# Optimization experiments

Hardware: AMD Instinct MI355X
Metric: run time of the kernel (lower is better)

The kernel has to match this reference:

```python
import jax, jax.numpy as jnp
import numpy as np

N_NODES = 100000
N_EDGES = 1600000
N_FEAT = 32
HIDDEN = 96
N_GRAPHS = 2048


def setup_inputs() -> dict:
    key = jax.random.key(0)
    ks = jax.random.split(key, 16)
    x = jax.random.normal(ks[0], (N_NODES, N_FEAT), dtype=jnp.float32)
    edge_index = jax.random.randint(ks[1], (2, N_EDGES), 0, N_NODES, dtype=jnp.int64)
    batch = jnp.sort(jax.random.randint(ks[2], (N_NODES,), 0, N_GRAPHS, dtype=jnp.int64))

    def glorot(k, shape):
        lim = np.sqrt(6.0 / (shape[0] + shape[1]))
        return jax.random.uniform(k, shape, dtype=jnp.float32, minval=-lim, maxval=lim)

    return {
        "x": x, "edge_index": edge_index, "batch": batch,
        "W1": glorot(ks[3], (N_FEAT, HIDDEN)), "b1": jnp.zeros((HIDDEN,), jnp.float32),
        "W2": glorot(ks[4], (HIDDEN, HIDDEN)), "b2": jnp.zeros((HIDDEN,), jnp.float32),
        "W3": glorot(ks[5], (HIDDEN, HIDDEN)), "b3": jnp.zeros((HIDDEN,), jnp.float32),
        "W4": glorot(ks[6], (HIDDEN, HIDDEN)), "b4": jnp.zeros((HIDDEN,), jnp.float32),
        "Wf1": glorot(ks[7], (HIDDEN, 32)), "bf1": jnp.zeros((32,), jnp.float32),
        "Wf2": glorot(ks[8], (32, 1)), "bf2": jnp.zeros((1,), jnp.float32),
    }


def _gcn_norm(edge_index, num_nodes):
    # PyG GCNConv default: add self-loops, symmetric normalization D^-1/2 (A+I) D^-1/2
    loops = jnp.arange(num_nodes, dtype=edge_index.dtype)
    src = jnp.concatenate([edge_index[0], loops])
    dst = jnp.concatenate([edge_index[1], loops])
    deg = jax.ops.segment_sum(jnp.ones_like(dst, dtype=jnp.float32), dst, num_segments=num_nodes)
    dinv = jnp.where(deg > 0, jax.lax.rsqrt(jnp.where(deg > 0, deg, 1.0)), 0.0)
    norm = dinv[src] * dinv[dst]  # [E + N]
    return src, dst, norm


def _gcn_conv(x, src, dst, norm, W, b, num_nodes):
    xw = x @ W                      # [N, out]
    msg = xw[src] * norm[:, None]   # [E+N, out] gather + scale
    out = jax.ops.segment_sum(msg, dst, num_segments=num_nodes)  # scatter-add
    return out + b


def reference(x, edge_index, batch, W1, b1, W2, b2, W3, b3, W4, b4, Wf1, bf1, Wf2, bf2):
    n = x.shape[0]
    src, dst, norm = _gcn_norm(edge_index, n)
    h = jax.nn.relu(_gcn_conv(x, src, dst, norm, W1, b1, n))
    h = jax.nn.relu(_gcn_conv(h, src, dst, norm, W2, b2, n))
    h = jax.nn.relu(_gcn_conv(h, src, dst, norm, W3, b3, n))
    h = jax.nn.relu(_gcn_conv(h, src, dst, norm, W4, b4, n))
    g = jax.ops.segment_sum(h, batch, num_segments=N_GRAPHS)  # global_add_pool [G, 96]
    g = jax.nn.relu(g @ Wf1 + bf1)
    return g @ Wf2 + bf2  # [G, 1]
```

## Files before the change

kernel.cpp:

```cpp
#include <hip/hip_runtime.h>
#include <hip/hip_fp16.h>


#define HIDDEN 96

__device__ inline float4 h4_to_f4(uint2 u) {
    __half2 a = *reinterpret_cast<__half2*>(&u.x);
    __half2 b = *reinterpret_cast<__half2*>(&u.y);
    float2 fa = __half22float2(a), fb = __half22float2(b);
    return make_float4(fa.x, fa.y, fb.x, fb.y);
}

__device__ inline uint2 f4_to_h4(float4 v) {
    __half2 a = __float22half2_rn(make_float2(v.x, v.y));
    __half2 b = __float22half2_rn(make_float2(v.z, v.w));
    uint2 u;
    u.x = *reinterpret_cast<unsigned*>(&a);
    u.y = *reinterpret_cast<unsigned*>(&b);
    return u;
}

__device__ inline int pad8(int c) { return (c + 7) & ~7; }

__global__ __launch_bounds__(256) void zero_int_kernel(int* p, int n) {
    int i = blockIdx.x * 256 + threadIdx.x;
    if (i < n) p[i] = 0;
}

__global__ __launch_bounds__(256) void zero_kernel(float* p, int n) {
    int i = blockIdx.x * 256 + threadIdx.x;
    if (i < n) p[i] = 0.0f;
}

__global__ __launch_bounds__(256) void cast_h_kernel(const float4* __restrict__ in,
                                                     uint2* __restrict__ out, int n4) {
    int i = blockIdx.x * 256 + threadIdx.x;
    if (i < n4) out[i] = f4_to_h4(in[i]);
}

__global__ __launch_bounds__(256) void deg_pos_kernel(const int* __restrict__ dst,
                                                      int* __restrict__ cnt,
                                                      int* __restrict__ epos, int E) {
    int e = blockIdx.x * 256 + threadIdx.x;
    if (e < E) epos[e] = atomicAdd(&cnt[dst[e]], 1);
}

__global__ __launch_bounds__(256) void dinv_kernel(const int* __restrict__ cnt,
                                                   float* __restrict__ dinv, int n) {
    int i = blockIdx.x * 256 + threadIdx.x;
    if (i < n) dinv[i] = rsqrtf((float)(cnt[i] + 1));
}

__global__ __launch_bounds__(256) void scan_reduce_kernel(const int* __restrict__ cnt,
                                                          int* __restrict__ bsum, int N) {
    __shared__ int s[256];
    int b = blockIdx.x, tid = threadIdx.x;
    int base = b * 1024;
    int v = 0;
    for (int j = tid; j < 1024; j += 256) {
        int i = base + j;
        v += (i < N) ? pad8(cnt[i]) : 0;
    }
    s[tid] = v;
    __syncthreads();
    for (int off = 128; off > 0; off >>= 1) {
        if (tid < off) s[tid] += s[tid + off];
        __syncthreads();
    }
    if (tid == 0) bsum[b] = s[0];
}

__global__ __launch_bounds__(128) void scan_bsum_kernel(int* __restrict__ bsum, int nb) {
    __shared__ int s[128];
    int tid = threadIdx.x;
    int v = (tid < nb) ? bsum[tid] : 0;
    s[tid] = v;
    __syncthreads();
    for (int off = 1; off < 128; off <<= 1) {
        int t = (tid >= off) ? s[tid - off] : 0;
        __syncthreads();
        s[tid] += t;
        __syncthreads();
    }
    if (tid < nb) bsum[tid] = s[tid] - v;
}

__global__ __launch_bounds__(256) void scan_write_kernel(const int* __restrict__ cnt,
                                                         const int* __restrict__ bsum,
                                                         int* __restrict__ rowptr, int N) {
    __shared__ int ts[256];
    int b = blockIdx.x, tid = threadIdx.x;
    int base = b * 1024 + tid * 4;
    int v0 = (base + 0 < N) ? pad8(cnt[base + 0]) : 0;
    int v1 = (base + 1 < N) ? pad8(cnt[base + 1]) : 0;
    int v2 = (base + 2 < N) ? pad8(cnt[base + 2]) : 0;
    int v3 = (base + 3 < N) ? pad8(cnt[base + 3]) : 0;
    int sum = v0 + v1 + v2 + v3;
    ts[tid] = sum;
    __syncthreads();
    for (int off = 1; off < 256; off <<= 1) {
        int t = (tid >= off) ? ts[tid - off] : 0;
        __syncthreads();
        ts[tid] += t;
        __syncthreads();
    }
    int excl = bsum[b] + ts[tid] - sum;
    if (base + 0 <= N) rowptr[base + 0] = excl;
    if (base + 1 <= N) rowptr[base + 1] = excl + v0;
    if (base + 2 <= N) rowptr[base + 2] = excl + v0 + v1;
    if (base + 3 <= N) rowptr[base + 3] = excl + v0 + v1 + v2;
}

__global__ __launch_bounds__(256) void fill_csr_kernel(const int* __restrict__ src,
                                                       const int* __restrict__ dst,
                                                       const int* __restrict__ epos,
                                                       const float* __restrict__ dinv,
                                                       const int* __restrict__ rowptr,
                                                       int* __restrict__ col,
                                                       float* __restrict__ val, int E) {
    int e = blockIdx.x * 256 + threadIdx.x;
    if (e >= E) return;
    int s = src[e];
    int d = dst[e];
    int idx = rowptr[d] + epos[e];
    col[idx] = s;
    val[idx] = dinv[s] * dinv[d];
}

template <int K, bool RELU, bool BIAS>
__global__ __launch_bounds__(256) void gemm_kernel(const uint2* __restrict__ X,
                                                   const float* __restrict__ W,
                                                   const float* __restrict__ b,
                                                   uint2* __restrict__ Y, int n) {
    __shared__ float wlds[K * HIDDEN];
    for (int idx = threadIdx.x; idx < K * HIDDEN; idx += 256) wlds[idx] = W[idx];
    __syncthreads();

    int row = blockIdx.x * 256 + threadIdx.x;
    if (row >= n) return;

    float4 acc[24];
#pragma unroll
    for (int j = 0; j < 24; j++) acc[j] = make_float4(0.f, 0.f, 0.f, 0.f);

    const float4* wl4 = reinterpret_cast<const float4*>(wlds);
    const uint2* xrow = X + (size_t)row * (K / 4);

    for (int k0 = 0; k0 < K; k0 += 4) {
        float4 xv = h4_to_f4(xrow[k0 >> 2]);
        if (RELU) {
            xv.x = fmaxf(xv.x, 0.f); xv.y = fmaxf(xv.y, 0.f);
            xv.z = fmaxf(xv.z, 0.f); xv.w = fmaxf(xv.w, 0.f);
        }
#pragma unroll
        for (int kk = 0; kk < 4; kk++) {
            float xs = (kk == 0) ? xv.x : (kk == 1) ? xv.y : (kk == 2) ? xv.z : xv.w;
#pragma unroll
            for (int j = 0; j < 24; j++) {
                float4 w = wl4[(k0 + kk) * 24 + j];
                acc[j].x += xs * w.x;
                acc[j].y += xs * w.y;
                acc[j].z += xs * w.z;
                acc[j].w += xs * w.w;
            }
        }
    }

    uint2* y2 = Y + (size_t)row * 24;
#pragma unroll
    for (int j = 0; j < 24; j++) {
        if (BIAS) {
            float4 bb = reinterpret_cast<const float4*>(b)[j];
            acc[j].x += bb.x; acc[j].y += bb.y; acc[j].z += bb.z; acc[j].w += bb.w;
        }
        y2[j] = f4_to_h4(acc[j]);
    }
}

template <int TPN, bool POOL, bool BIAS>
__global__ __launch_bounds__(256) void aggregate_kernel(const uint2* __restrict__ xwh,
                                                        const int* __restrict__ rowptr,
                                                        const int* __restrict__ col,
                                                        const float* __restrict__ val,
                                                        const float* __restrict__ dinv,
                                                        const float* __restrict__ b,
                                                        uint2* __restrict__ out,
                                                        const int* __restrict__ batch,
                                                        float* __restrict__ gpool, int n) {
    unsigned t = blockIdx.x * 256 + threadIdx.x;
    unsigned i = t / (unsigned)TPN, q = t % (unsigned)TPN;
    if (i >= (unsigned)n) return;

    float dv = dinv[i];
    float s = dv * dv;
    float4 self = h4_to_f4(xwh[i * TPN + q]);
    float4 acc = make_float4(s * self.x, s * self.y, s * self.z, s * self.w);
    if (BIAS) {
        float4 bb = reinterpret_cast<const float4*>(b)[q];
        acc.x += bb.x; acc.y += bb.y; acc.z += bb.z; acc.w += bb.w;
    }

    int e = rowptr[i], end = rowptr[i + 1];
    for (; e < end; e += 8) {
        int4 ca = *reinterpret_cast<const int4*>(col + e);
        int4 cb = *reinterpret_cast<const int4*>(col + e + 4);
        float4 wa = *reinterpret_cast<const float4*>(val + e);
        float4 wb = *reinterpret_cast<const float4*>(val + e + 4);
        uint2 u0 = xwh[(unsigned)ca.x * TPN + q];
        uint2 u1 = xwh[(unsigned)ca.y * TPN + q];
        uint2 u2 = xwh[(unsigned)ca.z * TPN + q];
        uint2 u3 = xwh[(unsigned)ca.w * TPN + q];
        uint2 u4 = xwh[(unsigned)cb.x * TPN + q];
        uint2 u5 = xwh[(unsigned)cb.y * TPN + q];
        uint2 u6 = xwh[(unsigned)cb.z * TPN + q];
        uint2 u7 = xwh[(unsigned)cb.w * TPN + q];
        float4 v0 = h4_to_f4(u0), v1 = h4_to_f4(u1);
        float4 v2 = h4_to_f4(u2), v3 = h4_to_f4(u3);
        float4 v4 = h4_to_f4(u4), v5 = h4_to_f4(u5);
        float4 v6 = h4_to_f4(u6), v7 = h4_to_f4(u7);
        acc.x += wa.x * v0.x + wa.y * v1.x + wa.z * v2.x + wa.w * v3.x
               + wb.x * v4.x + wb.y * v5.x + wb.z * v6.x + wb.w * v7.x;
        acc.y += wa.x * v0.y + wa.y * v1.y + wa.z * v2.y + wa.w * v3.y
               + wb.x * v4.y + wb.y * v5.y + wb.z * v6.y + wb.w * v7.y;
        acc.z += wa.x * v0.z + wa.y * v1.z + wa.z * v2.z + wa.w * v3.z
               + wb.x * v4.z + wb.y * v5.z + wb.z * v6.z + wb.w * v7.z;
        acc.w += wa.x * v0.w + wa.y * v1.w + wa.z * v2.w + wa.w * v3.w
               + wb.x * v4.w + wb.y * v5.w + wb.z * v6.w + wb.w * v7.w;
    }

    if (POOL) {
        float* o = gpool + (size_t)batch[i] * (TPN * 4);
        unsigned fo = q * 4u;
        atomicAdd(o + fo + 0, fmaxf(acc.x, 0.f));
        atomicAdd(o + fo + 1, fmaxf(acc.y, 0.f));
        atomicAdd(o + fo + 2, fmaxf(acc.z, 0.f));
        atomicAdd(o + fo + 3, fmaxf(acc.w, 0.f));
    } else {
        out[i * TPN + q] = f4_to_h4(acc);
    }
}

__global__ __launch_bounds__(64) void mlp_kernel(const float* __restrict__ g,
                                                 const float* __restrict__ Wf1,
                                                 const float* __restrict__ bf1,
                                                 const float* __restrict__ Wf2,
                                                 const float* __restrict__ bf2,
                                                 float* __restrict__ out, int G) {
    __shared__ float gs[HIDDEN];
    __shared__ float hid[32];
    int blk = blockIdx.x;
    int lane = threadIdx.x;
    for (int idx = lane; idx < HIDDEN; idx += 64) gs[idx] = g[(size_t)blk * HIDDEN + idx];
    __syncthreads();
    if (lane < 32) {
        float a = bf1[lane];
        for (int k = 0; k < HIDDEN; k++) a = fmaf(gs[k], Wf1[k * 32 + lane], a);
        hid[lane] = fmaxf(a, 0.f);
    }
    __syncthreads();
    if (lane == 0) {
        float o = bf2[0];
        for (int k = 0; k < 32; k++) o = fmaf(hid[k], Wf2[k], o);
        out[blk] = o;
    }
}

extern "C" void kernel_launch(void* const* d_in, const int* in_sizes, int n_in,
                              void* d_out, int out_size, void* d_ws, size_t ws_size,
                              hipStream_t stream) {
    const float* x     = (const float*)d_in[0];
    const int*   ei    = (const int*)d_in[1];
    const int*   batch = (const int*)d_in[2];
    const float* W1 = (const float*)d_in[3];  const float* b1 = (const float*)d_in[4];
    const float* W2 = (const float*)d_in[5];  const float* b2 = (const float*)d_in[6];
    const float* W3 = (const float*)d_in[7];  const float* b3 = (const float*)d_in[8];
    const float* W4 = (const float*)d_in[9];  const float* b4 = (const float*)d_in[10];
    const float* Wf1 = (const float*)d_in[11]; const float* bf1 = (const float*)d_in[12];
    const float* Wf2 = (const float*)d_in[13]; const float* bf2 = (const float*)d_in[14];
    float* out = (float*)d_out;

    int N = in_sizes[0] / 32;
    int E = in_sizes[1] / 2;
    int G = out_size;
    const int* src = ei;
    const int* dst = ei + E;
    int Emax = E + 8 * N;

    char* ws = (char*)d_ws;
    size_t off = 0;
    auto alloc = [&](size_t bytes) -> void* {
        void* p = (void*)(ws + off);
        off += (bytes + 255) & ~(size_t)255;
        return p;
    };
    int*   degcnt = (int*)alloc((size_t)N * 4);
    float* dinv   = (float*)alloc((size_t)N * 4);
    int*   rowptr = (int*)alloc((size_t)(N + 1) * 4);
    int*   bsum   = (int*)alloc((size_t)128 * 4);
    int*   col    = (int*)alloc((size_t)Emax * 4);
    float* val    = (float*)alloc((size_t)Emax * 4);
    int*   epos   = (int*)alloc((size_t)E * 4);
    uint2* xh     = (uint2*)alloc((size_t)N * 32 * 2);
    uint2* aggXh  = (uint2*)alloc((size_t)N * 32 * 2);
    uint2* bufB   = (uint2*)alloc((size_t)N * HIDDEN * 2);
    uint2* bufH   = (uint2*)alloc((size_t)N * HIDDEN * 2);
    float* gbuf   = (float*)alloc((size_t)G * HIDDEN * 4);
    (void)ws_size;

    int gN   = (N + 255) / 256;
    int gE   = (E + 255) / 256;
    int gEm  = (Emax + 255) / 256;
    int gAgg32 = (int)(((long long)N * 8 + 255) / 256);
    int gAgg96 = (int)(((long long)N * 24 + 255) / 256);
    int nb   = (N + 1023) / 1024;

    zero_int_kernel<<<gN, 256, 0, stream>>>(degcnt, N);
    zero_int_kernel<<<gEm, 256, 0, stream>>>(col, Emax);
    zero_kernel<<<gEm, 256, 0, stream>>>(val, Emax);
    deg_pos_kernel<<<gE, 256, 0, stream>>>(dst, degcnt, epos, E);
    dinv_kernel<<<gN, 256, 0, stream>>>(degcnt, dinv, N);
    scan_reduce_kernel<<<nb, 256, 0, stream>>>(degcnt, bsum, N);
    scan_bsum_kernel<<<1, 128, 0, stream>>>(bsum, nb);
    scan_write_kernel<<<nb, 256, 0, stream>>>(degcnt, bsum, rowptr, N);
    fill_csr_kernel<<<gE, 256, 0, stream>>>(src, dst, epos, dinv, rowptr, col, val, E);

    cast_h_kernel<<<(N * 8 + 255) / 256, 256, 0, stream>>>(
        reinterpret_cast<const float4*>(x), xh, N * 8);
    aggregate_kernel<8, false, false><<<gAgg32, 256, 0, stream>>>(
        xh, rowptr, col, val, dinv, nullptr, aggXh, nullptr, nullptr, N);
    gemm_kernel<32, false, true><<<gN, 256, 0, stream>>>(aggXh, W1, b1, bufB, N);

    gemm_kernel<96, true, false><<<gN, 256, 0, stream>>>(bufB, W2, nullptr, bufH, N);
    aggregate_kernel<24, false, true><<<gAgg96, 256, 0, stream>>>(
        bufH, rowptr, col, val, dinv, b2, bufB, nullptr, nullptr, N);

    gemm_kernel<96, true, false><<<gN, 256, 0, stream>>>(bufB, W3, nullptr, bufH, N);
    aggregate_kernel<24, false, true><<<gAgg96, 256, 0, stream>>>(
        bufH, rowptr, col, val, dinv, b3, bufB, nullptr, nullptr, N);

    zero_kernel<<<(G * HIDDEN + 255) / 256, 256, 0, stream>>>(gbuf, G * HIDDEN);
    gemm_kernel<96, true, false><<<gN, 256, 0, stream>>>(bufB, W4, nullptr, bufH, N);
    aggregate_kernel<24, true, true><<<gAgg96, 256, 0, stream>>>(
        bufH, rowptr, col, val, dinv, b4, nullptr, batch, gbuf, N);

    mlp_kernel<<<G, 64, 0, stream>>>(gbuf, Wf1, bf1, Wf2, bf2, out, G);
}
```

Baseline: 696.5 us.

## Widen aggregate gathers to 16-byte loads and pad CSR rows to 4

Result: slower. 922.0 us (+32.4%).

```diff
diff --git a/kernel.cpp b/kernel.cpp
--- a/kernel.cpp
+++ b/kernel.cpp
@@ -20,7 +20,7 @@
     return u;
 }
 
-__device__ inline int pad8(int c) { return (c + 7) & ~7; }
+__device__ inline int pad4(int c) { return (c + 3) & ~3; }
 
 __global__ __launch_bounds__(256) void zero_int_kernel(int* p, int n) {
     int i = blockIdx.x * 256 + threadIdx.x;
@@ -59,7 +59,7 @@
     int v = 0;
     for (int j = tid; j < 1024; j += 256) {
         int i = base + j;
-        v += (i < N) ? pad8(cnt[i]) : 0;
+        v += (i < N) ? pad4(cnt[i]) : 0;
     }
     s[tid] = v;
     __syncthreads();
@@ -91,10 +91,10 @@
     __shared__ int ts[256];
     int b = blockIdx.x, tid = threadIdx.x;
     int base = b * 1024 + tid * 4;
-    int v0 = (base + 0 < N) ? pad8(cnt[base + 0]) : 0;
-    int v1 = (base + 1 < N) ? pad8(cnt[base + 1]) : 0;
-    int v2 = (base + 2 < N) ? pad8(cnt[base + 2]) : 0;
-    int v3 = (base + 3 < N) ? pad8(cnt[base + 3]) : 0;
+    int v0 = (base + 0 < N) ? pad4(cnt[base + 0]) : 0;
+    int v1 = (base + 1 < N) ? pad4(cnt[base + 1]) : 0;
+    int v2 = (base + 2 < N) ? pad4(cnt[base + 2]) : 0;
+    int v3 = (base + 3 < N) ? pad4(cnt[base + 3]) : 0;
     int sum = v0 + v1 + v2 + v3;
     ts[tid] = sum;
     __syncthreads();
@@ -178,13 +178,13 @@
 }
 
 template <int TPN, bool POOL, bool BIAS>
-__global__ __launch_bounds__(256) void aggregate_kernel(const uint2* __restrict__ xwh,
+__global__ __launch_bounds__(256) void aggregate_kernel(const uint4* __restrict__ xwh,
                                                         const int* __restrict__ rowptr,
                                                         const int* __restrict__ col,
                                                         const float* __restrict__ val,
                                                         const float* __restrict__ dinv,
                                                         const float* __restrict__ b,
-                                                        uint2* __restrict__ out,
+                                                        uint4* __restrict__ out,
                                                         const int* __restrict__ batch,
                                                         float* __restrict__ gpool, int n) {
     unsigned t = blockIdx.x * 256 + threadIdx.x;
@@ -193,50 +193,53 @@
 
     float dv = dinv[i];
     float s = dv * dv;
-    float4 self = h4_to_f4(xwh[i * TPN + q]);
-    float4 acc = make_float4(s * self.x, s * self.y, s * self.z, s * self.w);
+    uint4 su = xwh[i * TPN + q];
+    float4 sa = h4_to_f4(make_uint2(su.x, su.y));
+    float4 sb = h4_to_f4(make_uint2(su.z, su.w));
+    float4 accA = make_float4(s * sa.x, s * sa.y, s * sa.z, s * sa.w);
+    float4 accB = make_float4(s * sb.x, s * sb.y, s * sb.z, s * sb.w);
     if (BIAS) {
-        float4 bb = reinterpret_cast<const float4*>(b)[q];
-        acc.x += bb.x; acc.y += bb.y; acc.z += bb.z; acc.w += bb.w;
+        const float4* b4 = reinterpret_cast<const float4*>(b);
+        float4 ba = b4[q * 2 + 0], bb = b4[q * 2 + 1];
+        accA.x += ba.x; accA.y += ba.y; accA.z += ba.z; accA.w += ba.w;
+        accB.x += bb.x; accB.y += bb.y; accB.z += bb.z; accB.w += bb.w;
     }
 
     int e = rowptr[i], end = rowptr[i + 1];
-    for (; e < end; e += 8) {
-        int4 ca = *reinterpret_cast<const int4*>(col + e);
-        int4 cb = *reinterpret_cast<const int4*>(col + e + 4);
-        float4 wa = *reinterpret_cast<const float4*>(val + e);
-        float4 wb = *reinterpret_cast<const float4*>(val + e + 4);
-        uint2 u0 = xwh[(unsigned)ca.x * TPN + q];
-        uint2 u1 = xwh[(unsigned)ca.y * TPN + q];
-        uint2 u2 = xwh[(unsigned)ca.z * TPN + q];
-        uint2 u3 = xwh[(unsigned)ca.w * TPN + q];
-        uint2 u4 = xwh[(unsigned)cb.x * TPN + q];
-        uint2 u5 = xwh[(unsigned)cb.y * TPN + q];
-        uint2 u6 = xwh[(unsigned)cb.z * TPN + q];
-        uint2 u7 = xwh[(unsigned)cb.w * TPN + q];
-        float4 v0 = h4_to_f4(u0), v1 = h4_to_f4(u1);
-        float4 v2 = h4_to_f4(u2), v3 = h4_to_f4(u3);
-        float4 v4 = h4_to_f4(u4), v5 = h4_to_f4(u5);
-        float4 v6 = h4_to_f4(u6), v7 = h4_to_f4(u7);
-        acc.x += wa.x * v0.x + wa.y * v1.x + wa.z * v2.x + wa.w * v3.x
-               + wb.x * v4.x + wb.y * v5.x + wb.z * v6.x + wb.w * v7.x;
-        acc.y += wa.x * v0.y + wa.y * v1.y + wa.z * v2.y + wa.w * v3.y
-               + wb.x * v4.y + wb.y * v5.y + wb.z * v6.y + wb.w * v7.y;
-        acc.z += wa.x * v0.z + wa.y * v1.z + wa.z * v2.z + wa.w * v3.z
-               + wb.x * v4.z + wb.y * v5.z + wb.z * v6.z + wb.w * v7.z;
-        acc.w += wa.x * v0.w + wa.y * v1.w + wa.z * v2.w + wa.w * v3.w
-               + wb.x * v4.w + wb.y * v5.w + wb.z * v6.w + wb.w * v7.w;
+    for (; e < end; e += 4) {
+        int4 c4 = *reinterpret_cast<const int4*>(col + e);
+        float4 w4 = *reinterpret_cast<const float4*>(val + e);
+        uint4 u0 = xwh[(unsigned)c4.x * TPN + q];
+        uint4 u1 = xwh[(unsigned)c4.y * TPN + q];
+        uint4 u2 = xwh[(unsigned)c4.z * TPN + q];
+        uint4 u3 = xwh[(unsigned)c4.w * TPN + q];
+        float4 a0 = h4_to_f4(make_uint2(u0.x, u0.y)), b0 = h4_to_f4(make_uint2(u0.z, u0.w));
+        float4 a1 = h4_to_f4(make_uint2(u1.x, u1.y)), b1 = h4_to_f4(make_uint2(u1.z, u1.w));
+        float4 a2 = h4_to_f4(make_uint2(u2.x, u2.y)), b2 = h4_to_f4(make_uint2(u2.z, u2.w));
+        float4 a3 = h4_to_f4(make_uint2(u3.x, u3.y)), b3 = h4_to_f4(make_uint2(u3.z, u3.w));
+        accA.x += w4.x * a0.x + w4.y * a1.x + w4.z * a2.x + w4.w * a3.x;
+        accA.y += w4.x * a0.y + w4.y * a1.y + w4.z * a2.y + w4.w * a3.y;
+        accA.z += w4.x * a0.z + w4.y * a1.z + w4.z * a2.z + w4.w * a3.z;
+        accA.w += w4.x * a0.w + w4.y * a1.w + w4.z * a2.w + w4.w * a3.w;
+        accB.x += w4.x * b0.x + w4.y * b1.x + w4.z * b2.x + w4.w * b3.x;
+        accB.y += w4.x * b0.y + w4.y * b1.y + w4.z * b2.y + w4.w * b3.y;
+        accB.z += w4.x * b0.z + w4.y * b1.z + w4.z * b2.z + w4.w * b3.z;
+        accB.w += w4.x * b0.w + w4.y * b1.w + w4.z * b2.w + w4.w * b3.w;
     }
 
     if (POOL) {
-        float* o = gpool + (size_t)batch[i] * (TPN * 4);
-        unsigned fo = q * 4u;
-        atomicAdd(o + fo + 0, fmaxf(acc.x, 0.f));
-        atomicAdd(o + fo + 1, fmaxf(acc.y, 0.f));
-        atomicAdd(o + fo + 2, fmaxf(acc.z, 0.f));
-        atomicAdd(o + fo + 3, fmaxf(acc.w, 0.f));
+        float* o = gpool + (size_t)batch[i] * (TPN * 8) + q * 8u;
+        atomicAdd(o + 0, fmaxf(accA.x, 0.f));
+        atomicAdd(o + 1, fmaxf(accA.y, 0.f));
+        atomicAdd(o + 2, fmaxf(accA.z, 0.f));
+        atomicAdd(o + 3, fmaxf(accA.w, 0.f));
+        atomicAdd(o + 4, fmaxf(accB.x, 0.f));
+        atomicAdd(o + 5, fmaxf(accB.y, 0.f));
+        atomicAdd(o + 6, fmaxf(accB.z, 0.f));
+        atomicAdd(o + 7, fmaxf(accB.w, 0.f));
     } else {
-        out[i * TPN + q] = f4_to_h4(acc);
+        uint2 ha = f4_to_h4(accA), hb = f4_to_h4(accB);
+        out[i * TPN + q] = make_uint4(ha.x, ha.y, hb.x, hb.y);
     }
 }
 
@@ -284,7 +287,7 @@
     int G = out_size;
     const int* src = ei;
     const int* dst = ei + E;
-    int Emax = E + 8 * N;
+    int Emax = E + 4 * N;
 
     char* ws = (char*)d_ws;
     size_t off = 0;
@@ -301,17 +304,17 @@
     float* val    = (float*)alloc((size_t)Emax * 4);
     int*   epos   = (int*)alloc((size_t)E * 4);
     uint2* xh     = (uint2*)alloc((size_t)N * 32 * 2);
-    uint2* aggXh  = (uint2*)alloc((size_t)N * 32 * 2);
-    uint2* bufB   = (uint2*)alloc((size_t)N * HIDDEN * 2);
-    uint2* bufH   = (uint2*)alloc((size_t)N * HIDDEN * 2);
+    uint4* aggXh  = (uint4*)alloc((size_t)N * 32 * 2);
+    uint4* bufB   = (uint4*)alloc((size_t)N * HIDDEN * 2);
+    uint4* bufH   = (uint4*)alloc((size_t)N * HIDDEN * 2);
     float* gbuf   = (float*)alloc((size_t)G * HIDDEN * 4);
     (void)ws_size;
 
     int gN   = (N + 255) / 256;
     int gE   = (E + 255) / 256;
     int gEm  = (Emax + 255) / 256;
-    int gAgg32 = (int)(((long long)N * 8 + 255) / 256);
-    int gAgg96 = (int)(((long long)N * 24 + 255) / 256);
+    int gAgg32 = (int)(((long long)N * 4 + 255) / 256);
+    int gAgg96 = (int)(((long long)N * 12 + 255) / 256);
     int nb   = (N + 1023) / 1024;
 
     zero_int_kernel<<<gN, 256, 0, stream>>>(degcnt, N);
@@ -326,21 +329,30 @@
 
     cast_h_kernel<<<(N * 8 + 255) / 256, 256, 0, stream>>>(
         reinterpret_cast<const float4*>(x), xh, N * 8);
-    aggregate_kernel<8, false, false><<<gAgg32, 256, 0, stream>>>(
-        xh, rowptr, col, val, dinv, nullptr, aggXh, nullptr, nullptr, N);
-    gemm_kernel<32, false, true><<<gN, 256, 0, stream>>>(aggXh, W1, b1, bufB, N);
-
-    gemm_kernel<96, true, false><<<gN, 256, 0, stream>>>(bufB, W2, nullptr, bufH, N);
-    aggregate_kernel<24, false, true><<<gAgg96, 256, 0, stream>>>(
+    aggregate_kernel<4, false, false><<<gAgg32, 256, 0, stream>>>(
+        reinterpret_cast<const uint4*>(xh), rowptr, col, val, dinv, nullptr,
+        aggXh, nullptr, nullptr, N);
+    gemm_kernel<32, false, true><<<gN, 256, 0, stream>>>(
+        reinterpret_cast<const uint2*>(aggXh), W1, b1,
+        reinterpret_cast<uint2*>(bufB), N);
+
+    gemm_kernel<96, true, false><<<gN, 256, 0, stream>>>(
+        reinterpret_cast<const uint2*>(bufB), W2, nullptr,
+        reinterpret_cast<uint2*>(bufH), N);
+    aggregate_kernel<12, false, true><<<gAgg96, 256, 0, stream>>>(
         bufH, rowptr, col, val, dinv, b2, bufB, nullptr, nullptr, N);
 
-    gemm_kernel<96, true, false><<<gN, 256, 0, stream>>>(bufB, W3, nullptr, bufH, N);
-    aggregate_kernel<24, false, true><<<gAgg96, 256, 0, stream>>>(
+    gemm_kernel<96, true, false><<<gN, 256, 0, stream>>>(
+        reinterpret_cast<const uint2*>(bufB), W3, nullptr,
+        reinterpret_cast<uint2*>(bufH), N);
+    aggregate_kernel<12, false, true><<<gAgg96, 256, 0, stream>>>(
         bufH, rowptr, col, val, dinv, b3, bufB, nullptr, nullptr, N);
 
     zero_kernel<<<(G * HIDDEN + 255) / 256, 256, 0, stream>>>(gbuf, G * HIDDEN);
-    gemm_kernel<96, true, false><<<gN, 256, 0, stream>>>(bufB, W4, nullptr, bufH, N);
-    aggregate_kernel<24, true, true><<<gAgg96, 256, 0, stream>>>(
+    gemm_kernel<96, true, false><<<gN, 256, 0, stream>>>(
+        reinterpret_cast<const uint2*>(bufB), W4, nullptr,
+        reinterpret_cast<uint2*>(bufH), N);
+    aggregate_kernel<12, true, true><<<gAgg96, 256, 0, stream>>>(
         bufH, rowptr, col, val, dinv, b4, nullptr, batch, gbuf, N);
 
     mlp_kernel<<<G, 64, 0, stream>>>(gbuf, Wf1, bf1, Wf2, bf2, out, G);
```

## Sort nodes into degree buckets so aggregation warps process similar-degree rows

Applied to the files above, without the earlier changes.

Measured after the change: 1.461 ms. +109.8%, slower.

```diff
diff --git a/kernel.cpp b/kernel.cpp
--- a/kernel.cpp
+++ b/kernel.cpp
@@ -20,7 +20,7 @@
     return u;
 }
 
-__device__ inline int pad8(int c) { return (c + 7) & ~7; }
+__device__ inline int pad8i(int c) { return (c + 7) & ~7; }
 
 __global__ __launch_bounds__(256) void zero_int_kernel(int* p, int n) {
     int i = blockIdx.x * 256 + threadIdx.x;
@@ -51,15 +51,50 @@
     if (i < n) dinv[i] = rsqrtf((float)(cnt[i] + 1));
 }
 
+__global__ __launch_bounds__(256) void bucket_kernel(const int* __restrict__ cnt,
+                                                     int* __restrict__ hist,
+                                                     int* __restrict__ mypos, int N) {
+    int i = blockIdx.x * 256 + threadIdx.x;
+    if (i >= N) return;
+    int k = min(pad8i(cnt[i]) >> 3, 63);
+    mypos[i] = atomicAdd(&hist[k], 1);
+}
+
+__global__ __launch_bounds__(64) void hist_scan_kernel(const int* __restrict__ hist,
+                                                       int* __restrict__ base) {
+    int tid = threadIdx.x;
+    int h = hist[tid];
+    int v = h;
+    for (int off = 1; off < 64; off <<= 1) {
+        int t = __shfl_up(v, off);
+        if (tid >= off) v += t;
+    }
+    base[tid] = v - h;
+}
+
+__global__ __launch_bounds__(256) void rank_kernel(const int* __restrict__ cnt,
+                                                   const int* __restrict__ base,
+                                                   const int* __restrict__ mypos,
+                                                   int* __restrict__ rank,
+                                                   int* __restrict__ perm, int N) {
+    int i = blockIdx.x * 256 + threadIdx.x;
+    if (i >= N) return;
+    int k = min(pad8i(cnt[i]) >> 3, 63);
+    int r = base[k] + mypos[i];
+    rank[i] = r;
+    perm[r] = i;
+}
+
 __global__ __launch_bounds__(256) void scan_reduce_kernel(const int* __restrict__ cnt,
+                                                          const int* __restrict__ perm,
                                                           int* __restrict__ bsum, int N) {
     __shared__ int s[256];
     int b = blockIdx.x, tid = threadIdx.x;
-    int base = b * 1024;
+    int basei = b * 1024;
     int v = 0;
     for (int j = tid; j < 1024; j += 256) {
-        int i = base + j;
-        v += (i < N) ? pad8(cnt[i]) : 0;
+        int i = basei + j;
+        v += (i < N) ? pad8i(cnt[perm[i]]) : 0;
     }
     s[tid] = v;
     __syncthreads();
@@ -86,15 +121,16 @@
 }
 
 __global__ __launch_bounds__(256) void scan_write_kernel(const int* __restrict__ cnt,
+                                                         const int* __restrict__ perm,
                                                          const int* __restrict__ bsum,
                                                          int* __restrict__ rowptr, int N) {
     __shared__ int ts[256];
     int b = blockIdx.x, tid = threadIdx.x;
-    int base = b * 1024 + tid * 4;
-    int v0 = (base + 0 < N) ? pad8(cnt[base + 0]) : 0;
-    int v1 = (base + 1 < N) ? pad8(cnt[base + 1]) : 0;
-    int v2 = (base + 2 < N) ? pad8(cnt[base + 2]) : 0;
-    int v3 = (base + 3 < N) ? pad8(cnt[base + 3]) : 0;
+    int basei = b * 1024 + tid * 4;
+    int v0 = (basei + 0 < N) ? pad8i(cnt[perm[basei + 0]]) : 0;
+    int v1 = (basei + 1 < N) ? pad8i(cnt[perm[basei + 1]]) : 0;
+    int v2 = (basei + 2 < N) ? pad8i(cnt[perm[basei + 2]]) : 0;
+    int v3 = (basei + 3 < N) ? pad8i(cnt[perm[basei + 3]]) : 0;
     int sum = v0 + v1 + v2 + v3;
     ts[tid] = sum;
     __syncthreads();
@@ -105,15 +141,16 @@
         __syncthreads();
     }
     int excl = bsum[b] + ts[tid] - sum;
-    if (base + 0 <= N) rowptr[base + 0] = excl;
-    if (base + 1 <= N) rowptr[base + 1] = excl + v0;
-    if (base + 2 <= N) rowptr[base + 2] = excl + v0 + v1;
-    if (base + 3 <= N) rowptr[base + 3] = excl + v0 + v1 + v2;
+    if (basei + 0 <= N) rowptr[basei + 0] = excl;
+    if (basei + 1 <= N) rowptr[basei + 1] = excl + v0;
+    if (basei + 2 <= N) rowptr[basei + 2] = excl + v0 + v1;
+    if (basei + 3 <= N) rowptr[basei + 3] = excl + v0 + v1 + v2;
 }
 
 __global__ __launch_bounds__(256) void fill_csr_kernel(const int* __restrict__ src,
                                                        const int* __restrict__ dst,
                                                        const int* __restrict__ epos,
+                                                       const int* __restrict__ rank,
                                                        const float* __restrict__ dinv,
                                                        const int* __restrict__ rowptr,
                                                        int* __restrict__ col,
@@ -122,7 +159,7 @@
     if (e >= E) return;
     int s = src[e];
     int d = dst[e];
-    int idx = rowptr[d] + epos[e];
+    int idx = rowptr[rank[d]] + epos[e];
     col[idx] = s;
     val[idx] = dinv[s] * dinv[d];
 }
@@ -182,14 +219,16 @@
                                                         const int* __restrict__ rowptr,
                                                         const int* __restrict__ col,
                                                         const float* __restrict__ val,
+                                                        const int* __restrict__ perm,
                                                         const float* __restrict__ dinv,
                                                         const float* __restrict__ b,
                                                         uint2* __restrict__ out,
                                                         const int* __restrict__ batch,
                                                         float* __restrict__ gpool, int n) {
     unsigned t = blockIdx.x * 256 + threadIdx.x;
-    unsigned i = t / (unsigned)TPN, q = t % (unsigned)TPN;
-    if (i >= (unsigned)n) return;
+    unsigned j = t / (unsigned)TPN, q = t % (unsigned)TPN;
+    if (j >= (unsigned)n) return;
+    unsigned i = (unsigned)perm[j];
 
     float dv = dinv[i];
     float s = dv * dv;
@@ -200,7 +239,7 @@
         acc.x += bb.x; acc.y += bb.y; acc.z += bb.z; acc.w += bb.w;
     }
 
-    int e = rowptr[i], end = rowptr[i + 1];
+    int e = rowptr[j], end = rowptr[j + 1];
     for (; e < end; e += 8) {
         int4 ca = *reinterpret_cast<const int4*>(col + e);
         int4 cb = *reinterpret_cast<const int4*>(col + e + 4);
@@ -297,6 +336,11 @@
     float* dinv   = (float*)alloc((size_t)N * 4);
     int*   rowptr = (int*)alloc((size_t)(N + 1) * 4);
     int*   bsum   = (int*)alloc((size_t)128 * 4);
+    int*   hist   = (int*)alloc((size_t)64 * 4);
+    int*   hbase  = (int*)alloc((size_t)64 * 4);
+    int*   mypos  = (int*)alloc((size_t)N * 4);
+    int*   rankb  = (int*)alloc((size_t)N * 4);
+    int*   perm   = (int*)alloc((size_t)N * 4);
     int*   col    = (int*)alloc((size_t)Emax * 4);
     float* val    = (float*)alloc((size_t)Emax * 4);
     int*   epos   = (int*)alloc((size_t)E * 4);
@@ -315,33 +359,37 @@
     int nb   = (N + 1023) / 1024;
 
     zero_int_kernel<<<gN, 256, 0, stream>>>(degcnt, N);
+    zero_int_kernel<<<1, 256, 0, stream>>>(hist, 64);
     zero_int_kernel<<<gEm, 256, 0, stream>>>(col, Emax);
     zero_kernel<<<gEm, 256, 0, stream>>>(val, Emax);
     deg_pos_kernel<<<gE, 256, 0, stream>>>(dst, degcnt, epos, E);
     dinv_kernel<<<gN, 256, 0, stream>>>(degcnt, dinv, N);
-    scan_reduce_kernel<<<nb, 256, 0, stream>>>(degcnt, bsum, N);
+    bucket_kernel<<<gN, 256, 0, stream>>>(degcnt, hist, mypos, N);
+    hist_scan_kernel<<<1, 64, 0, stream>>>(hist, hbase);
+    rank_kernel<<<gN, 256, 0, stream>>>(degcnt, hbase, mypos, rankb, perm, N);
+    scan_reduce_kernel<<<nb, 256, 0, stream>>>(degcnt, perm, bsum, N);
     scan_bsum_kernel<<<1, 128, 0, stream>>>(bsum, nb);
-    scan_write_kernel<<<nb, 256, 0, stream>>>(degcnt, bsum, rowptr, N);
-    fill_csr_kernel<<<gE, 256, 0, stream>>>(src, dst, epos, dinv, rowptr, col, val, E);
+    scan_write_kernel<<<nb, 256, 0, stream>>>(degcnt, perm, bsum, rowptr, N);
+    fill_csr_kernel<<<gE, 256, 0, stream>>>(src, dst, epos, rankb, dinv, rowptr, col, val, E);
 
     cast_h_kernel<<<(N * 8 + 255) / 256, 256, 0, stream>>>(
         reinterpret_cast<const float4*>(x), xh, N * 8);
     aggregate_kernel<8, false, false><<<gAgg32, 256, 0, stream>>>(
-        xh, rowptr, col, val, dinv, nullptr, aggXh, nullptr, nullptr, N);
+        xh, rowptr, col, val, perm, dinv, nullptr, aggXh, nullptr, nullptr, N);
     gemm_kernel<32, false, true><<<gN, 256, 0, stream>>>(aggXh, W1, b1, bufB, N);
 
     gemm_kernel<96, true, false><<<gN, 256, 0, stream>>>(bufB, W2, nullptr, bufH, N);
     aggregate_kernel<24, false, true><<<gAgg96, 256, 0, stream>>>(
-        bufH, rowptr, col, val, dinv, b2, bufB, nullptr, nullptr, N);
+        bufH, rowptr, col, val, perm, dinv, b2, bufB, nullptr, nullptr, N);
 
     gemm_kernel<96, true, false><<<gN, 256, 0, stream>>>(bufB, W3, nullptr, bufH, N);
     aggregate_kernel<24, false, true><<<gAgg96, 256, 0, stream>>>(
-        bufH, rowptr, col, val, dinv, b3, bufB, nullptr, nullptr, N);
+        bufH, rowptr, col, val, perm, dinv, b3, bufB, nullptr, nullptr, N);
 
     zero_kernel<<<(G * HIDDEN + 255) / 256, 256, 0, stream>>>(gbuf, G * HIDDEN);
     gemm_kernel<96, true, false><<<gN, 256, 0, stream>>>(bufB, W4, nullptr, bufH, N);
     aggregate_kernel<24, true, true><<<gAgg96, 256, 0, stream>>>(
-        bufH, rowptr, col, val, dinv, b4, nullptr, batch, gbuf, N);
+        bufH, rowptr, col, val, perm, dinv, b4, nullptr, batch, gbuf, N);
 
     mlp_kernel<<<G, 64, 0, stream>>>(gbuf, Wf1, bf1, Wf2, bf2, out, G);
 }
```
